# Kernel tuning notes

Hardware: AMD Instinct MI355X
Metric: run time of the kernel (lower is better)

Reference implementation:

```python
import jax, jax.numpy as jnp
import numpy as np

HIDDEN = 2048
NUM_HEADS = 16
KEY_DIM = 1024      # hidden * expand_k (0.5)
VALUE_DIM = 2048    # hidden * expand_v (1.0)
HEAD_K = KEY_DIM // NUM_HEADS   # 64
HEAD_V = VALUE_DIM // NUM_HEADS # 128
EPS = 1e-5
B, T = 8, 4096


def _rmsnorm(x, w, eps=EPS):
    var = jnp.mean(jnp.square(x), axis=-1, keepdims=True)
    return x * jax.lax.rsqrt(var + eps) * w


def setup_inputs() -> dict:
    key = jax.random.key(0)
    ks = jax.random.split(key, 7)
    s = 1.0 / np.sqrt(HIDDEN)
    return {
        "hidden_states": jax.random.normal(ks[0], (B, T, HIDDEN), dtype=jnp.float32),
        "recurrent_state": jax.random.normal(ks[1], (B, NUM_HEADS, HEAD_K, HEAD_V), dtype=jnp.float32),
        "norm_w": jnp.ones((HIDDEN,), dtype=jnp.float32),
        "q_w": jax.random.uniform(ks[2], (KEY_DIM, HIDDEN), jnp.float32, -s, s),
        "v_norm_w": jnp.ones((HEAD_V,), dtype=jnp.float32),
        "o_w": jax.random.uniform(ks[3], (HIDDEN, VALUE_DIM), jnp.float32, -s, s),
        "gate_w": jax.random.uniform(ks[4], (HIDDEN, HIDDEN), jnp.float32, -s, s),
    }


def reference(hidden_states, recurrent_state, norm_w, q_w, v_norm_w, o_w, gate_w):
    x = _rmsnorm(hidden_states, norm_w)                       # (B,T,D)
    q = x @ q_w.T                                             # (B,T,KEY_DIM)
    q = q.reshape(*q.shape[:2], NUM_HEADS, HEAD_K)            # (B,T,H,K)
    # L2 normalize along last dim (F.normalize default eps=1e-12 on the norm)
    norm = jnp.maximum(jnp.linalg.norm(q, axis=-1, keepdims=True), 1e-12)
    q = q / norm
    o = jnp.einsum('bthk,bhkv->bthv', q, recurrent_state)     # (B,T,H,V)
    o = _rmsnorm(o, v_norm_w)
    o = o.reshape(*o.shape[:2], VALUE_DIM)                    # (B,T,VALUE_DIM)
    o = o @ o_w.T                                             # (B,T,D)
    gate = jax.nn.sigmoid(x @ gate_w.T)                       # (B,T,D)
    return gate * o
```

## Files before the change

kernel.cpp:

```cpp
#include <hip/hip_runtime.h>

typedef unsigned short u16;
typedef unsigned int u32;
typedef __attribute__((ext_vector_type(4))) float f32x4;
typedef __attribute__((ext_vector_type(8))) short short8;
typedef __attribute__((ext_vector_type(4))) short short4v;

#define HIDDEN 2048
#define NHEADS 16
#define KEYDIM 1024
#define VALDIM 2048
#define HEADK 64
#define HEADV 128
#define NBATCH 8
#define SEQ 4096
#define NTOK (NBATCH * SEQ)

__device__ __forceinline__ u16 f2bf(float f) {
  union { float f; u32 u; } c; c.f = f;
  u32 r = c.u + 0x7FFFu + ((c.u >> 16) & 1u);
  return (u16)(r >> 16);
}
__device__ __forceinline__ float bf2f(u16 h) {
  union { u32 u; float f; } c; c.u = ((u32)h) << 16;
  return c.f;
}

__global__ __launch_bounds__(256) void cast_bf16_k(const float* __restrict__ in,
                                                   u16* __restrict__ out, int n4) {
  int i = blockIdx.x * blockDim.x + threadIdx.x;
  if (i >= n4) return;
  f32x4 v = *(const f32x4*)(in + (size_t)i * 4);
  short4v o;
  o[0] = (short)f2bf(v[0]); o[1] = (short)f2bf(v[1]);
  o[2] = (short)f2bf(v[2]); o[3] = (short)f2bf(v[3]);
  *(short4v*)(out + (size_t)i * 4) = o;
}

__global__ __launch_bounds__(256) void rmsnorm_cast_k(const float* __restrict__ x,
                                                      const float* __restrict__ w,
                                                      u16* __restrict__ xb) {
  int r = blockIdx.x;
  int tid = threadIdx.x;
  const float* xp = x + (size_t)r * HIDDEN + tid * 8;
  f32x4 v0 = *(const f32x4*)xp;
  f32x4 v1 = *(const f32x4*)(xp + 4);
  float ss = v0[0]*v0[0]+v0[1]*v0[1]+v0[2]*v0[2]+v0[3]*v0[3]
           + v1[0]*v1[0]+v1[1]*v1[1]+v1[2]*v1[2]+v1[3]*v1[3];
  #pragma unroll
  for (int m = 32; m >= 1; m >>= 1) ss += __shfl_xor(ss, m);
  __shared__ float red[4];
  if ((tid & 63) == 0) red[tid >> 6] = ss;
  __syncthreads();
  float tot = red[0] + red[1] + red[2] + red[3];
  float inv = rsqrtf(tot * (1.0f / HIDDEN) + 1e-5f);
  const float* wp = w + tid * 8;
  f32x4 w0 = *(const f32x4*)wp;
  f32x4 w1 = *(const f32x4*)(wp + 4);
  short8 o;
  o[0] = (short)f2bf(v0[0] * inv * w0[0]);
  o[1] = (short)f2bf(v0[1] * inv * w0[1]);
  o[2] = (short)f2bf(v0[2] * inv * w0[2]);
  o[3] = (short)f2bf(v0[3] * inv * w0[3]);
  o[4] = (short)f2bf(v1[0] * inv * w1[0]);
  o[5] = (short)f2bf(v1[1] * inv * w1[1]);
  o[6] = (short)f2bf(v1[2] * inv * w1[2]);
  o[7] = (short)f2bf(v1[3] * inv * w1[3]);
  *(short8*)(xb + (size_t)r * HIDDEN + tid * 8) = o;
}


__device__ __forceinline__ void gload16(const u16* g, u16* l) {
  __builtin_amdgcn_global_load_lds((const __attribute__((address_space(1))) void*)g,
                                   (__attribute__((address_space(3))) void*)l, 16, 0, 0);
}

#define BAR()                                  \
  do {                                         \
    asm volatile("" ::: "memory");             \
    __builtin_amdgcn_s_barrier();              \
    asm volatile("" ::: "memory");             \
  } while (0)

template <int MODE>
__global__ __launch_bounds__(512, 2) void gemm1b_k(const u16* __restrict__ A,
                                                   const u16* __restrict__ Bw,
                                                   void* __restrict__ Cptr,
                                                   u16* __restrict__ Aux,
                                                   int M, int N, int K) {
  extern __shared__ u16 lds[];
  const int tid = threadIdx.x;
  const int wid = tid >> 6;
  const int wm = wid >> 2;
  const int wn = wid & 3;
  const int l = tid & 63;
  const int lr = l & 15;
  const int kq = l >> 4;

  const int ntn = N >> 8;
  const int per = gridDim.x >> 3;
  const int b = blockIdx.x;
  const int sidx = (b & 7) * per + (b >> 3);
  const int mt = sidx / ntn;
  const int nt = sidx - mt * ntn;

  const u16* Ag = A + (size_t)(mt * 256) * K;
  const u16* Bg = Bw + (size_t)(nt * 256) * K;

  const int srow = tid >> 3;
  const int schunk = (tid & 7) ^ (srow & 7);

#define STAGE_A(c, h)                                                          \
  do {                                                                         \
    const u16* _s = Ag + (size_t)((h) * 128 + srow) * K + ((c) << 6) + schunk * 8; \
    u16* _d = lds + (((c) & 1) << 15) + (h) * 8192 + tid * 8;                  \
    gload16(_s, _d);                                                           \
    gload16(_s + (size_t)64 * K, _d + 4096);                                   \
  } while (0)
#define STAGE_B(c, h)                                                          \
  do {                                                                         \
    const u16* _s = Bg + (size_t)((h) * 128 + srow) * K + ((c) << 6) + schunk * 8; \
    u16* _d = lds + (((c) & 1) << 15) + 16384 + (h) * 8192 + tid * 8;          \
    gload16(_s, _d);                                                           \
    gload16(_s + (size_t)64 * K, _d + 4096);                                   \
  } while (0)

  const int c0s = (kq ^ (lr & 7)) << 3;
  const int c1s = ((4 + kq) ^ (lr & 7)) << 3;
  const int aRowBase = (wm * 128 + lr) * 64;
  const int bRowBase = (wn * 64 + lr) * 64;

  short8 afr[4][2];
  short8 bfr[2][2][2];
  f32x4 acc[8][4] = {};

  auto LDA = [&](int buf, int mh) {
    #pragma unroll
    for (int mi = 0; mi < 4; ++mi) {
      const u16* p = lds + (buf << 15) + aRowBase + (mh * 64 + mi * 16) * 64;
      afr[mi][0] = *(const short8*)(p + c0s);
      afr[mi][1] = *(const short8*)(p + c1s);
    }
  };
  auto LDB_ALL = [&](int buf) {
    #pragma unroll
    for (int nh = 0; nh < 2; ++nh) {
      #pragma unroll
      for (int ni = 0; ni < 2; ++ni) {
        const u16* p = lds + (buf << 15) + 16384 + bRowBase + ((nh * 2 + ni) * 16) * 64;
        bfr[nh][ni][0] = *(const short8*)(p + c0s);
        bfr[nh][ni][1] = *(const short8*)(p + c1s);
      }
    }
  };
  auto MMA = [&](int mh, int nh) {
    __builtin_amdgcn_s_setprio(1);
    #pragma unroll
    for (int mi = 0; mi < 4; ++mi) {
      #pragma unroll
      for (int ni = 0; ni < 2; ++ni) {
        int m = mh * 4 + mi, n = nh * 2 + ni;
        acc[m][n] = __builtin_amdgcn_mfma_f32_16x16x32_bf16(afr[mi][0], bfr[nh][ni][0], acc[m][n], 0, 0, 0);
        acc[m][n] = __builtin_amdgcn_mfma_f32_16x16x32_bf16(afr[mi][1], bfr[nh][ni][1], acc[m][n], 0, 0, 0);
      }
    }
    __builtin_amdgcn_s_setprio(0);
  };

  STAGE_A(0, 0); STAGE_A(0, 1);
  STAGE_B(0, 0); STAGE_B(0, 1);
  STAGE_B(1, 0); STAGE_B(1, 1);
  asm volatile("s_waitcnt vmcnt(4)" ::: "memory");
  BAR();

  const int NITER = K >> 7;
  for (int i = 0; i < NITER; ++i) {
    const int g = (i + 1 < NITER);
    const int cA = 2 * i + 1, c2 = 2 * i + 2, c3 = 2 * i + 3;

    LDB_ALL(0); LDA(0, 0);
    STAGE_A(cA, 0);
    BAR(); MMA(0, 0);
    STAGE_A(cA, 1);
    BAR(); MMA(0, 1);
    LDA(0, 1);
    if (g) STAGE_B(c2, 0);
    BAR(); MMA(1, 1);
    if (g) {
      STAGE_B(c2, 1);
      asm volatile("s_waitcnt vmcnt(4)" ::: "memory");
    } else {
      asm volatile("s_waitcnt vmcnt(0)" ::: "memory");
    }
    BAR(); MMA(1, 0);

    LDB_ALL(1); LDA(1, 0);
    if (g) STAGE_A(c2, 0);
    BAR(); MMA(0, 0);
    if (g) STAGE_A(c2, 1);
    BAR(); MMA(0, 1);
    LDA(1, 1);
    if (g) STAGE_B(c3, 0);
    BAR(); MMA(1, 1);
    if (g) {
      STAGE_B(c3, 1);
      asm volatile("s_waitcnt vmcnt(4)" ::: "memory");
    }
    BAR(); MMA(1, 0);
  }
#undef STAGE_A
#undef STAGE_B

  const int rowB = mt * 256 + wm * 128 + kq * 4;
  const int colB = nt * 256 + wn * 64 + lr;
  #pragma unroll
  for (int m = 0; m < 8; ++m) {
    #pragma unroll
    for (int n = 0; n < 4; ++n) {
      #pragma unroll
      for (int j = 0; j < 4; ++j) {
        int row = rowB + m * 16 + j;
        int col = colB + n * 16;
        float v = acc[m][n][j];
        if constexpr (MODE == 2) {
          size_t idx = (size_t)row * N + col;
          ((float*)Cptr)[idx] = v * bf2f(Aux[idx]);
        } else if constexpr (MODE == 4) {
          size_t idx = (size_t)row * N + col;
          float* O = (float*)Cptr;
          O[idx] = O[idx] * v;
        } else {
          if (nt < 4) {
            int h = col >> 6, k = col & 63;
            int bb = row >> 12, tok = row & (SEQ - 1);
            Aux[((size_t)(bb * NHEADS + h) * SEQ + tok) * HEADK + k] = f2bf(v);
          } else {
            int colg = col - 1024;
            float sg = 1.0f / (1.0f + __expf(-v));
            if constexpr (MODE == 5) {
              ((u16*)Cptr)[(size_t)row * HIDDEN + colg] = f2bf(sg);
            } else {
              ((float*)Cptr)[(size_t)row * HIDDEN + colg] = sg;
            }
          }
        }
      }
    }
  }
}

__global__ __launch_bounds__(256) void glaread_k(const u16* __restrict__ qT,
                                                 const float* __restrict__ S,
                                                 const float* __restrict__ vw,
                                                 u16* __restrict__ omid) {
  int bh = blockIdx.x;
  int b = bh >> 4, h = bh & 15;
  int tid = threadIdx.x;
  int w = tid >> 6, l = tid & 63;
  int lr = l & 15, kq = l >> 4;

  __shared__ u16 tile[4][16 * 136];

  const float* Sp = S + (size_t)bh * HEADK * HEADV;
  short8 bfrag[8][2];
  #pragma unroll
  for (int n = 0; n < 8; ++n) {
    #pragma unroll
    for (int s = 0; s < 2; ++s) {
      #pragma unroll
      for (int i = 0; i < 8; ++i)
        bfrag[n][s][i] =
            (short)f2bf(Sp[(size_t)(s * 32 + kq * 8 + i) * HEADV + n * 16 + lr]);
    }
  }
  float vwn[8];
  #pragma unroll
  for (int n = 0; n < 8; ++n) vwn[n] = vw[n * 16 + lr];

  const u16* qbase = qT + (size_t)bh * SEQ * HEADK;
  const int ttk = l >> 2;
  const int cc = (l & 3) * 32;

  #pragma unroll 1
  for (int it = 0; it < 8; ++it) {
    int t0 = blockIdx.y * 512 + it * 64 + w * 16;
    const u16* qp = qbase + (size_t)(t0 + lr) * HEADK;
    short8 a0 = *(const short8*)(qp + kq * 8);
    short8 a1 = *(const short8*)(qp + 32 + kq * 8);

    float ss = 0.f;
    #pragma unroll
    for (int i = 0; i < 8; ++i) {
      float x0 = bf2f((u16)a0[i]), x1 = bf2f((u16)a1[i]);
      ss += x0 * x0 + x1 * x1;
    }
    ss += __shfl_xor(ss, 16);
    ss += __shfl_xor(ss, 32);
    float sc = 1.0f / fmaxf(sqrtf(ss), 1e-12f);

    short8 an0, an1;
    #pragma unroll
    for (int i = 0; i < 8; ++i) {
      an0[i] = (short)f2bf(bf2f((u16)a0[i]) * sc);
      an1[i] = (short)f2bf(bf2f((u16)a1[i]) * sc);
    }

    f32x4 acc[8] = {};
    #pragma unroll
    for (int n = 0; n < 8; ++n) {
      acc[n] = __builtin_amdgcn_mfma_f32_16x16x32_bf16(an0, bfrag[n][0], acc[n], 0, 0, 0);
      acc[n] = __builtin_amdgcn_mfma_f32_16x16x32_bf16(an1, bfrag[n][1], acc[n], 0, 0, 0);
    }

    float part[4] = {0.f, 0.f, 0.f, 0.f};
    #pragma unroll
    for (int n = 0; n < 8; ++n) {
      #pragma unroll
      for (int j = 0; j < 4; ++j) part[j] += acc[n][j] * acc[n][j];
    }
    #pragma unroll
    for (int msk = 1; msk <= 8; msk <<= 1) {
      #pragma unroll
      for (int j = 0; j < 4; ++j) part[j] += __shfl_xor(part[j], msk);
    }
    #pragma unroll
    for (int j = 0; j < 4; ++j) {
      float inv = rsqrtf(part[j] * (1.0f / HEADV) + 1e-5f);
      #pragma unroll
      for (int n = 0; n < 8; ++n)
        tile[w][(kq * 4 + j) * 136 + n * 16 + lr] = f2bf(acc[n][j] * inv * vwn[n]);
    }
    asm volatile("s_waitcnt lgkmcnt(0)" ::: "memory");
    {
      const u16* src = &tile[w][ttk * 136 + cc];
      u16* dst = omid + (size_t)(b * SEQ + t0 + ttk) * VALDIM + h * HEADV + cc;
      short8 r0 = *(const short8*)(src);
      short8 r1 = *(const short8*)(src + 8);
      short8 r2 = *(const short8*)(src + 16);
      short8 r3 = *(const short8*)(src + 24);
      *(short8*)(dst) = r0;
      *(short8*)(dst + 8) = r1;
      *(short8*)(dst + 16) = r2;
      *(short8*)(dst + 24) = r3;
    }
    asm volatile("" ::: "memory");
  }
}

extern "C" void kernel_launch(void* const* d_in, const int* in_sizes, int n_in,
                              void* d_out, int out_size, void* d_ws, size_t ws_size,
                              hipStream_t stream) {
  const float* hs = (const float*)d_in[0];
  const float* S  = (const float*)d_in[1];
  const float* nw = (const float*)d_in[2];
  const float* qw = (const float*)d_in[3];
  const float* vw = (const float*)d_in[4];
  const float* ow = (const float*)d_in[5];
  const float* gw = (const float*)d_in[6];
  float* out = (float*)d_out;

  u16* xb   = (u16*)d_ws;
  u16* qT   = xb + (size_t)NTOK * HIDDEN;
  u16* qwb  = qT + (size_t)NTOK * KEYDIM;
  u16* gwb  = qwb + (size_t)KEYDIM * HIDDEN;
  u16* owb  = gwb + (size_t)HIDDEN * HIDDEN;
  u16* gatebuf = owb + (size_t)HIDDEN * VALDIM;
  u16* omid = xb;

  const size_t need = ((size_t)NTOK * HIDDEN * 2) * 2 + (size_t)NTOK * KEYDIM * 2 +
                      ((size_t)KEYDIM * HIDDEN + 2 * (size_t)HIDDEN * HIDDEN) * 2;
  const bool bigws = ws_size >= need;

  const size_t LDSB = 131072;

  cast_bf16_k<<<(KEYDIM * HIDDEN / 4 + 255) / 256, 256, 0, stream>>>(qw, qwb, KEYDIM * HIDDEN / 4);
  cast_bf16_k<<<(HIDDEN * HIDDEN / 4 + 255) / 256, 256, 0, stream>>>(gw, gwb, HIDDEN * HIDDEN / 4);
  cast_bf16_k<<<(HIDDEN * VALDIM / 4 + 255) / 256, 256, 0, stream>>>(ow, owb, HIDDEN * VALDIM / 4);

  rmsnorm_cast_k<<<NTOK, 256, 0, stream>>>(hs, nw, xb);

  if (bigws) {
    gemm1b_k<5><<<dim3((NTOK / 256) * ((KEYDIM + HIDDEN) / 256)), 512, LDSB, stream>>>(
        xb, qwb, gatebuf, qT, NTOK, KEYDIM + HIDDEN, HIDDEN);
  } else {
    gemm1b_k<6><<<dim3((NTOK / 256) * ((KEYDIM + HIDDEN) / 256)), 512, LDSB, stream>>>(
        xb, qwb, out, qT, NTOK, KEYDIM + HIDDEN, HIDDEN);
  }

  glaread_k<<<dim3(NBATCH * NHEADS, SEQ / 512), 256, 0, stream>>>(qT, S, vw, omid);

  if (bigws) {
    gemm1b_k<2><<<dim3((NTOK / 256) * (HIDDEN / 256)), 512, LDSB, stream>>>(
        omid, owb, out, gatebuf, NTOK, HIDDEN, VALDIM);
  } else {
    gemm1b_k<4><<<dim3((NTOK / 256) * (HIDDEN / 256)), 512, LDSB, stream>>>(
        omid, owb, out, nullptr, NTOK, HIDDEN, VALDIM);
  }
}
```

Baseline: 822.3 us.

## Replace 256x256 double-buffered GEMM with 128x256 triple-buffered K=32 pipeline

The main GEMM kernel moves from a 256x256 output tile with K=64 double buffering to a 128x256 tile with K=32 steps and a three-deep LDS ring buffer. LDS per block drops from 128KB to 72KB, and launch bounds ask for 4 blocks per CU. Each wave now holds a 4x4 accumulator grid, half the previous size. The aim is higher occupancy and smoother load/compute overlap, at the cost of less operand reuse per tile and more barriers per unit of K.

```diff
diff --git a/kernel.cpp b/kernel.cpp
--- a/kernel.cpp
+++ b/kernel.cpp
@@ -83,7 +83,7 @@
   } while (0)
 
 template <int MODE>
-__global__ __launch_bounds__(512, 2) void gemm1b_k(const u16* __restrict__ A,
+__global__ __launch_bounds__(512, 4) void gemm2b_k(const u16* __restrict__ A,
                                                    const u16* __restrict__ Bw,
                                                    void* __restrict__ Cptr,
                                                    u16* __restrict__ Aux,
@@ -104,117 +104,91 @@
   const int mt = sidx / ntn;
   const int nt = sidx - mt * ntn;
 
-  const u16* Ag = A + (size_t)(mt * 256) * K;
+  const u16* Ag = A + (size_t)(mt * 128) * K;
   const u16* Bg = Bw + (size_t)(nt * 256) * K;
 
-  const int srow = tid >> 3;
-  const int schunk = (tid & 7) ^ (srow & 7);
-
-#define STAGE_A(c, h)                                                          \
-  do {                                                                         \
-    const u16* _s = Ag + (size_t)((h) * 128 + srow) * K + ((c) << 6) + schunk * 8; \
-    u16* _d = lds + (((c) & 1) << 15) + (h) * 8192 + tid * 8;                  \
-    gload16(_s, _d);                                                           \
-    gload16(_s + (size_t)64 * K, _d + 4096);                                   \
+  const int srow = tid >> 2;
+  const int kel = (((tid & 3) ^ ((tid >> 3) & 3)) << 3);
+
+#define BUFB(c) (((c) % 3) * 12288)
+#define STAGE(c)                                                      \
+  do {                                                                \
+    const u16* _sa = Ag + (size_t)srow * K + ((c) << 5) + kel;        \
+    u16* _d = lds + BUFB(c) + tid * 8;                                \
+    gload16(_sa, _d);                                                 \
+    const u16* _sb = Bg + (size_t)srow * K + ((c) << 5) + kel;        \
+    gload16(_sb, _d + 4096);                                          \
+    gload16(_sb + (size_t)128 * K, _d + 8192);                        \
   } while (0)
-#define STAGE_B(c, h)                                                          \
-  do {                                                                         \
-    const u16* _s = Bg + (size_t)((h) * 128 + srow) * K + ((c) << 6) + schunk * 8; \
-    u16* _d = lds + (((c) & 1) << 15) + 16384 + (h) * 8192 + tid * 8;          \
-    gload16(_s, _d);                                                           \
-    gload16(_s + (size_t)64 * K, _d + 4096);                                   \
-  } while (0)
-
-  const int c0s = (kq ^ (lr & 7)) << 3;
-  const int c1s = ((4 + kq) ^ (lr & 7)) << 3;
-  const int aRowBase = (wm * 128 + lr) * 64;
-  const int bRowBase = (wn * 64 + lr) * 64;
-
-  short8 afr[4][2];
-  short8 bfr[2][2][2];
-  f32x4 acc[8][4] = {};
-
-  auto LDA = [&](int buf, int mh) {
+
+  int aoff[2][4], boff[4];
+  #pragma unroll
+  for (int mh = 0; mh < 2; ++mh) {
     #pragma unroll
     for (int mi = 0; mi < 4; ++mi) {
-      const u16* p = lds + (buf << 15) + aRowBase + (mh * 64 + mi * 16) * 64;
-      afr[mi][0] = *(const short8*)(p + c0s);
-      afr[mi][1] = *(const short8*)(p + c1s);
-    }
-  };
-  auto LDB_ALL = [&](int buf) {
-    #pragma unroll
-    for (int nh = 0; nh < 2; ++nh) {
-      #pragma unroll
-      for (int ni = 0; ni < 2; ++ni) {
-        const u16* p = lds + (buf << 15) + 16384 + bRowBase + ((nh * 2 + ni) * 16) * 64;
-        bfr[nh][ni][0] = *(const short8*)(p + c0s);
-        bfr[nh][ni][1] = *(const short8*)(p + c1s);
-      }
-    }
-  };
-  auto MMA = [&](int mh, int nh) {
+      int R = wm * 64 + mh * 0 + mi * 16 + lr;
+      (void)R;
+    }
+  }
+  #pragma unroll
+  for (int mi = 0; mi < 4; ++mi) {
+    int R = wm * 64 + mi * 16 + lr;
+    aoff[0][mi] = R * 32 + ((kq ^ ((R >> 1) & 3)) << 3);
+  }
+  #pragma unroll
+  for (int n = 0; n < 4; ++n) {
+    int R = wn * 64 + n * 16 + lr;
+    boff[n] = 4096 + R * 32 + ((kq ^ ((R >> 1) & 3)) << 3);
+  }
+
+  short8 afr[4], bfr[4];
+  f32x4 acc[4][4] = {};
+
+  STAGE(0);
+  STAGE(1);
+  asm volatile("s_waitcnt vmcnt(3)" ::: "memory");
+  BAR();
+
+  const int NT = K >> 5;
+  #pragma unroll 1
+  for (int c = 0; c < NT; ++c) {
+    const u16* bufT = lds + BUFB(c);
+    const int g2 = (c + 2 < NT);
+
+    #pragma unroll
+    for (int mi = 0; mi < 4; ++mi) afr[mi] = *(const short8*)(bufT + aoff[0][mi]);
+    bfr[0] = *(const short8*)(bufT + boff[0]);
+    bfr[1] = *(const short8*)(bufT + boff[1]);
+    if (g2) STAGE(c + 2);
+    BAR();
     __builtin_amdgcn_s_setprio(1);
     #pragma unroll
     for (int mi = 0; mi < 4; ++mi) {
-      #pragma unroll
-      for (int ni = 0; ni < 2; ++ni) {
-        int m = mh * 4 + mi, n = nh * 2 + ni;
-        acc[m][n] = __builtin_amdgcn_mfma_f32_16x16x32_bf16(afr[mi][0], bfr[nh][ni][0], acc[m][n], 0, 0, 0);
-        acc[m][n] = __builtin_amdgcn_mfma_f32_16x16x32_bf16(afr[mi][1], bfr[nh][ni][1], acc[m][n], 0, 0, 0);
-      }
+      acc[mi][0] = __builtin_amdgcn_mfma_f32_16x16x32_bf16(afr[mi], bfr[0], acc[mi][0], 0, 0, 0);
+      acc[mi][1] = __builtin_amdgcn_mfma_f32_16x16x32_bf16(afr[mi], bfr[1], acc[mi][1], 0, 0, 0);
     }
     __builtin_amdgcn_s_setprio(0);
-  };
-
-  STAGE_A(0, 0); STAGE_A(0, 1);
-  STAGE_B(0, 0); STAGE_B(0, 1);
-  STAGE_B(1, 0); STAGE_B(1, 1);
-  asm volatile("s_waitcnt vmcnt(4)" ::: "memory");
-  BAR();
-
-  const int NITER = K >> 7;
-  for (int i = 0; i < NITER; ++i) {
-    const int g = (i + 1 < NITER);
-    const int cA = 2 * i + 1, c2 = 2 * i + 2, c3 = 2 * i + 3;
-
-    LDB_ALL(0); LDA(0, 0);
-    STAGE_A(cA, 0);
-    BAR(); MMA(0, 0);
-    STAGE_A(cA, 1);
-    BAR(); MMA(0, 1);
-    LDA(0, 1);
-    if (g) STAGE_B(c2, 0);
-    BAR(); MMA(1, 1);
-    if (g) {
-      STAGE_B(c2, 1);
-      asm volatile("s_waitcnt vmcnt(4)" ::: "memory");
-    } else {
-      asm volatile("s_waitcnt vmcnt(0)" ::: "memory");
-    }
-    BAR(); MMA(1, 0);
-
-    LDB_ALL(1); LDA(1, 0);
-    if (g) STAGE_A(c2, 0);
-    BAR(); MMA(0, 0);
-    if (g) STAGE_A(c2, 1);
-    BAR(); MMA(0, 1);
-    LDA(1, 1);
-    if (g) STAGE_B(c3, 0);
-    BAR(); MMA(1, 1);
-    if (g) {
-      STAGE_B(c3, 1);
-      asm volatile("s_waitcnt vmcnt(4)" ::: "memory");
-    }
-    BAR(); MMA(1, 0);
-  }
-#undef STAGE_A
-#undef STAGE_B
-
-  const int rowB = mt * 256 + wm * 128 + kq * 4;
+
+    bfr[2] = *(const short8*)(bufT + boff[2]);
+    bfr[3] = *(const short8*)(bufT + boff[3]);
+    if (g2)              asm volatile("s_waitcnt vmcnt(3)" ::: "memory");
+    else if (c + 1 < NT) asm volatile("s_waitcnt vmcnt(0)" ::: "memory");
+    BAR();
+    __builtin_amdgcn_s_setprio(1);
+    #pragma unroll
+    for (int mi = 0; mi < 4; ++mi) {
+      acc[mi][2] = __builtin_amdgcn_mfma_f32_16x16x32_bf16(afr[mi], bfr[2], acc[mi][2], 0, 0, 0);
+      acc[mi][3] = __builtin_amdgcn_mfma_f32_16x16x32_bf16(afr[mi], bfr[3], acc[mi][3], 0, 0, 0);
+    }
+    __builtin_amdgcn_s_setprio(0);
+  }
+#undef STAGE
+#undef BUFB
+
+  const int rowB = mt * 128 + wm * 64 + kq * 4;
   const int colB = nt * 256 + wn * 64 + lr;
   #pragma unroll
-  for (int m = 0; m < 8; ++m) {
+  for (int m = 0; m < 4; ++m) {
     #pragma unroll
     for (int n = 0; n < 4; ++n) {
       #pragma unroll
@@ -371,7 +345,7 @@
                       ((size_t)KEYDIM * HIDDEN + 2 * (size_t)HIDDEN * HIDDEN) * 2;
   const bool bigws = ws_size >= need;
 
-  const size_t LDSB = 131072;
+  const size_t LDSB = 73728;
 
   cast_bf16_k<<<(KEYDIM * HIDDEN / 4 + 255) / 256, 256, 0, stream>>>(qw, qwb, KEYDIM * HIDDEN / 4);
   cast_bf16_k<<<(HIDDEN * HIDDEN / 4 + 255) / 256, 256, 0, stream>>>(gw, gwb, HIDDEN * HIDDEN / 4);
@@ -380,20 +354,20 @@
   rmsnorm_cast_k<<<NTOK, 256, 0, stream>>>(hs, nw, xb);
 
   if (bigws) {
-    gemm1b_k<5><<<dim3((NTOK / 256) * ((KEYDIM + HIDDEN) / 256)), 512, LDSB, stream>>>(
+    gemm2b_k<5><<<dim3((NTOK / 128) * ((KEYDIM + HIDDEN) / 256)), 512, LDSB, stream>>>(
         xb, qwb, gatebuf, qT, NTOK, KEYDIM + HIDDEN, HIDDEN);
   } else {
-    gemm1b_k<6><<<dim3((NTOK / 256) * ((KEYDIM + HIDDEN) / 256)), 512, LDSB, stream>>>(
+    gemm2b_k<6><<<dim3((NTOK / 128) * ((KEYDIM + HIDDEN) / 256)), 512, LDSB, stream>>>(
         xb, qwb, out, qT, NTOK, KEYDIM + HIDDEN, HIDDEN);
   }
 
   glaread_k<<<dim3(NBATCH * NHEADS, SEQ / 512), 256, 0, stream>>>(qT, S, vw, omid);
 
   if (bigws) {
-    gemm1b_k<2><<<dim3((NTOK / 256) * (HIDDEN / 256)), 512, LDSB, stream>>>(
+    gemm2b_k<2><<<dim3((NTOK / 128) * (HIDDEN / 256)), 512, LDSB, stream>>>(
         omid, owb, out, gatebuf, NTOK, HIDDEN, VALDIM);
   } else {
-    gemm1b_k<4><<<dim3((NTOK / 256) * (HIDDEN / 256)), 512, LDSB, stream>>>(
+    gemm2b_k<4><<<dim3((NTOK / 128) * (HIDDEN / 256)), 512, LDSB, stream>>>(
         omid, owb, out, nullptr, NTOK, HIDDEN, VALDIM);
   }
 }
```

New measurement: 937.1 us. 1.14x slower.
